# Optimization experiments

Measured on AMD Instinct MI355X. Metric: run time of the kernel, lower is better.

## Reference

```python
import jax, jax.numpy as jnp
import numpy as np

B, H, W = 256, 256, 256
MIN_ = 100          # bg seeds sampled per image
MAX_ = 100          # fg seeds sampled per image
MIN_P = 0.1         # fraction of lowest-cam pixels forming bg candidate pool
FG_ERODE_K = 11
FG_ERODE_ITER = 1
KSZ = 3             # dilation kernel
IGNORE = -255


def setup_inputs() -> dict:
    key = jax.random.key(0)
    x = jax.random.uniform(key, (B, 1, H, W), dtype=jnp.float32)  # CAMs in [0,1)
    return {"x": x}


def _minpool(m, k):
    # kornia-style binary erosion with ones kernel == min-pool, SAME padding
    return jax.lax.reduce_window(m, jnp.inf, jax.lax.min, (1, k, k), (1, 1, 1), 'SAME')


def _maxpool(m, k):
    # kornia-style binary dilation with ones kernel == max-pool, SAME padding
    return jax.lax.reduce_window(m, -jnp.inf, jax.lax.max, (1, k, k), (1, 1, 1), 'SAME')


def _otsu(hist):
    # hist: (b,256) float32; returns per-sample Otsu threshold in [0,255]
    bc = jnp.arange(256, dtype=jnp.float32)
    w1 = jnp.cumsum(hist, -1)
    total = w1[:, -1:]
    w2 = total - w1 + hist                      # reverse cumulative weight
    s1 = jnp.cumsum(hist * bc, -1)
    s2 = s1[:, -1:] - s1 + hist * bc
    m1 = s1 / jnp.maximum(w1, 1.0)
    m2 = s2 / jnp.maximum(w2, 1.0)
    var12 = w1[:, :-1] * w2[:, 1:] * (m1[:, :-1] - m2[:, 1:]) ** 2
    return bc[jnp.argmax(var12, axis=-1)]        # (b,)


def reference(x):
    b, _, h, w = x.shape
    hw = h * w
    cam = x[:, 0]                                # (b,h,w)
    cam255 = jnp.floor(cam * 255.0)
    ci = jnp.clip(cam255, 0, 255).astype(jnp.int32).reshape(b, hw)

    hist = jax.vmap(lambda v: jnp.bincount(v, length=256))(ci).astype(jnp.float32)
    th = _otsu(hist)                              # (b,)
    th = jnp.where(th <= 0.0, 1.0, jnp.where(th >= 255.0, 254.0, th))
    bad = (ci.max(-1) == ci.min(-1))              # degenerate CAM -> no seeds

    # ----- fg: threshold, erode, uniform sample w/o replacement (Gumbel top-k) -----
    roi = (cam255 > th[:, None, None]).astype(jnp.float32)
    for _ in range(FG_ERODE_ITER):
        roi = _minpool(roi, FG_ERODE_K)
    roi_f = roi.reshape(b, hw)

    key = jax.random.key(42)
    kf, kb = jax.random.split(key)
    neg = jnp.float32(-jnp.inf)
    rows = jnp.arange(b)[:, None]

    sc_fg = jnp.where(roi_f > 0, jax.random.uniform(kf, (b, hw)), neg)
    v_fg, i_fg = jax.lax.top_k(sc_fg, MAX_)       # picks min(MAX_, n_fg) pixels
    fg = jnp.zeros((b, hw), jnp.float32).at[rows, i_fg].set(
        jnp.isfinite(v_fg).astype(jnp.float32))

    # ----- bg: lowest nbr_bg cam pixels are candidates; sample MIN_ of them -----
    nbr_bg = int(MIN_P * h * w)
    order = jnp.argsort(cam.reshape(b, hw), axis=-1)  # ascending
    cand = jnp.zeros((b, hw), jnp.float32).at[rows, order[:, :nbr_bg]].set(1.0)
    sc_bg = jnp.where(cand > 0, jax.random.uniform(kb, (b, hw)), neg)
    v_bg, i_bg = jax.lax.top_k(sc_bg, MIN_)
    bg = jnp.zeros((b, hw), jnp.float32).at[rows, i_bg].set(
        jnp.isfinite(v_bg).astype(jnp.float32))

    keep = (~bad)[:, None].astype(jnp.float32)
    fg = (fg * keep).reshape(b, h, w)
    bg = (bg * keep).reshape(b, h, w)

    # ----- dilate seeds, drop conflicts, assemble label map -----
    fg = _maxpool(fg, KSZ)
    bg = _maxpool(bg, KSZ)
    conflict = (fg + bg) >= 2.0
    fg = jnp.where(conflict, 0.0, fg)
    bg = jnp.where(conflict, 0.0, bg)

    out = jnp.full((b, h, w), IGNORE, jnp.int32)
    out = jnp.where(fg == 1.0, 1, out)
    out = jnp.where(bg == 1.0, 0, out)
    return out
```

## Files before the change

kernel.cpp:

```cpp
#include <hip/hip_runtime.h>
#include <stdint.h>

#define PARTITIONABLE 1

typedef unsigned int u32;
typedef unsigned long long u64;
typedef __attribute__((ext_vector_type(4))) int int4v;

static constexpr int BB  = 256;
static constexpr int HWN = 65536;
static constexpr u32 K_BG = 6553;
static constexpr u32 TOPK = 100;
static constexpr u32 CAP  = 7936;
static constexpr u32 FG_CAP = 1024;

static constexpr int OFF_LST   = 0;
static constexpr int OFF_FVL   = 0;
static constexpr int OFF_BVL   = 8192;
static constexpr int OFF_FHL   = 16384;
static constexpr int OFF_BHL   = 24576;
static constexpr int OFF_CIMG  = 63488;
static constexpr int OFF_FGL   = 63488;
static constexpr int OFF_SEEDB = 71680;
static constexpr int OFF_SEEDF = 79872;
static constexpr int OFF_HIST  = 129024;
static constexpr int OFF_HROWS = 137216;
static constexpr int OFF_ROWS  = 145408;
static constexpr int OFF_HO    = 153600;
static constexpr int OFF_EQ    = 154624;
static constexpr int OFF_SCAL  = 155648;
static constexpr int ARENA_BYTES = 155776;

__host__ __device__ inline u32 rotl32(u32 x, int d) { return (x << d) | (x >> (32 - d)); }

#define TF_ROUND(r) do { x0 += x1; x1 = rotl32(x1, r); x1 ^= x0; } while (0)

__host__ __device__ inline void threefry2x32(u32 k0, u32 k1, u32 x0, u32 x1, u32& o0, u32& o1) {
  u32 ks2 = k0 ^ k1 ^ 0x1BD11BDAu;
  x0 += k0; x1 += k1;
  TF_ROUND(13); TF_ROUND(15); TF_ROUND(26); TF_ROUND(6);
  x0 += k1;  x1 += ks2 + 1u;
  TF_ROUND(17); TF_ROUND(29); TF_ROUND(16); TF_ROUND(24);
  x0 += ks2; x1 += k0 + 2u;
  TF_ROUND(13); TF_ROUND(15); TF_ROUND(26); TF_ROUND(6);
  x0 += k0;  x1 += k1 + 3u;
  TF_ROUND(17); TF_ROUND(29); TF_ROUND(16); TF_ROUND(24);
  x0 += k1;  x1 += ks2 + 4u;
  TF_ROUND(13); TF_ROUND(15); TF_ROUND(26); TF_ROUND(6);
  x0 += ks2; x1 += k0 + 5u;
  o0 = x0; o1 = x1;
}

__device__ inline u32 score_bits(u32 k0, u32 k1, u32 i) {
#if PARTITIONABLE
  u32 a, b;
  threefry2x32(k0, k1, 0u, i, a, b);
  return a ^ b;
#else
  const u32 HALF = 1u << 23;
  u32 a, b;
  if (i < HALF) { threefry2x32(k0, k1, i, i + HALF, a, b); return a; }
  threefry2x32(k0, k1, i - HALF, i, a, b); return b;
#endif
}

__device__ __forceinline__ u32 wscan_incl(u32 v, int lane) {
#pragma unroll
  for (int d = 1; d < 64; d <<= 1) { u32 t = __shfl_up(v, d, 64); if (lane >= d) v += t; }
  return v;
}

template<int BPT, int NT>
__device__ __forceinline__ void pselA(const u32* hist, u32* ws, int t, u32* h, u32& loc, u32& inc) {
  int lane = t & 63;
  loc = 0;
#pragma unroll
  for (int j = 0; j < BPT; j++) { h[j] = hist[BPT * t + j]; loc += h[j]; }
  inc = wscan_incl(loc, lane);
  if (lane == 63) ws[t >> 6] = inc;
}
template<int BPT, int NT>
__device__ __forceinline__ void pselB(u32 K, bool desc, const u32* ws, u32* sc, int t, const u32* h, u32 loc, u32 inc) {
  const int NW = NT / 64;
  int wid = t >> 6;
  u32 off = 0, total = 0;
#pragma unroll
  for (int k = 0; k < NW; k++) { u32 wv = ws[k]; total += wv; if (k < wid) off += wv; }
  inc += off;
  if (!desc) {
    u32 ex = inc - loc;
#pragma unroll
    for (int j = 0; j < BPT; j++) { if (ex < K && K <= ex + h[j]) { sc[0] = BPT * t + j; sc[1] = K - ex; } ex += h[j]; }
  } else {
    u32 ex = total - inc;
#pragma unroll
    for (int j = BPT - 1; j >= 0; j--) { if (ex < K && K <= ex + h[j]) { sc[0] = BPT * t + j; sc[1] = K - ex; } ex += h[j]; }
  }
}

template<int BPT, int NT>
__device__ void psel_full(u32* hist, u32 K, bool desc, u32* ws, u32* sc, int zeroN, int tid) {
  u32 h[BPT], loc = 0, inc = 0;
  bool act = tid < NT;
  if (act) pselA<BPT, NT>(hist, ws, tid, h, loc, inc);
  __syncthreads();
  if (act) pselB<BPT, NT>(K, desc, ws, sc, tid, h, loc, inc);
  for (int k = tid; k < zeroN; k += 1024) hist[k] = 0;
  __syncthreads();
}

__device__ __forceinline__ void otsu_wave0(const u32* hO, u32* scal, int lane) {
  u32 base = (u32)lane * 4;
  u32 h[4], cw[4], cs[4];
#pragma unroll
  for (int j = 0; j < 4; j++) h[j] = hO[base + j];
  cw[0] = h[0]; cs[0] = h[0] * base;
#pragma unroll
  for (int j = 1; j < 4; j++) { cw[j] = cw[j-1] + h[j]; cs[j] = cs[j-1] + h[j] * (base + j); }
  u32 incW = wscan_incl(cw[3], lane);
  u32 incS = wscan_incl(cs[3], lane);
  u32 offW = incW - cw[3], offS = incS - cs[3];
  u32 totW = __shfl(incW, 63, 64), totS = __shfl(incS, 63, 64);
  int nz = 0;
#pragma unroll
  for (int j = 0; j < 4; j++) nz += (h[j] != 0);
#pragma unroll
  for (int d = 1; d < 64; d <<= 1) nz += __shfl_xor(nz, d, 64);
  u32 selfW0 = cw[0] + offW, selfS0 = cs[0] + offS;
  u32 nxtW = __shfl_down(selfW0, 1, 64);
  u32 nxtS = __shfl_down(selfS0, 1, 64);
  u32 nxtH = __shfl_down(h[0], 1, 64);
  float total = (float)totW, stot = (float)totS;
  unsigned long long best = 0ull;
#pragma unroll
  for (int j = 0; j < 4; j++) {
    int t = (int)base + j;
    if (t < 255) {
      float h1 = (float)((j < 3) ? h[j+1] : nxtH);
      float w1 = (float)(cw[j] + offW);
      float w1n = (j < 3) ? (float)(cw[j+1] + offW) : (float)nxtW;
      float s1 = (float)(cs[j] + offS);
      float s1n = (j < 3) ? (float)(cs[j+1] + offS) : (float)nxtS;
      float w2 = total - w1n + h1;
      float s2 = stot - s1n + h1 * (float)(t + 1);
      float m1 = s1 / fmaxf(w1, 1.0f);
      float m2 = s2 / fmaxf(w2, 1.0f);
      float d = m1 - m2;
      float v = (w1 * w2) * (d * d);
      unsigned long long key = ((unsigned long long)__float_as_uint(v) << 32) | (u32)(255 - t);
      if (key > best) best = key;
    }
  }
#pragma unroll
  for (int d = 1; d < 64; d <<= 1) { unsigned long long o = __shfl_xor(best, d, 64); if (o > best) best = o; }
  if (lane == 0) {
    int bi = 255 - (int)(best & 0xFFFFFFFFu);
    float th = (float)bi;
    th = (th <= 0.0f) ? 1.0f : ((th >= 255.0f) ? 254.0f : th);
    scal[8] = (u32)(int)th;
    scal[5] = (nz <= 1) ? 1u : 0u;
  }
}

__device__ __forceinline__ void roi_bits(const u32* cImgW, u64* rows, u32 thiU, int tid) {
  u64 bits = 0;
#pragma unroll
  for (int k2 = 0; k2 < 16; k2++) {
    int k = (k2 + (tid >> 1)) & 15;
    u32 v4 = cImgW[tid * 16 + k];
    u32 m = 0;
    if ((v4 & 0xFFu) > thiU)         m |= 1u;
    if (((v4 >> 8) & 0xFFu) > thiU)  m |= 2u;
    if (((v4 >> 16) & 0xFFu) > thiU) m |= 4u;
    if ((v4 >> 24) > thiU)           m |= 8u;
    bits |= (u64)m << (4 * k);
  }
  rows[tid] = bits;
}

__device__ __forceinline__ void erode_h(const u64* rows, u64* hrows, int r) {
  u64 wv[4], h0[4];
  for (int j = 0; j < 4; j++) { wv[j] = rows[r * 4 + j]; h0[j] = wv[j]; }
  for (int s = 1; s <= 5; s++)
    for (int j = 0; j < 4; j++) {
      u64 hi = (j < 3) ? wv[j + 1] : ~0ull;
      u64 lo = (j > 0) ? wv[j - 1] : ~0ull;
      h0[j] &= ((wv[j] >> s) | (hi << (64 - s))) & ((wv[j] << s) | (lo >> (64 - s)));
    }
  for (int j = 0; j < 4; j++) hrows[r * 4 + j] = h0[j];
}

__device__ __forceinline__ void erode_v(const u64* hrows, u64* rows, int r) {
  u64 res[4] = {hrows[r * 4], hrows[r * 4 + 1], hrows[r * 4 + 2], hrows[r * 4 + 3]};
  for (int dr = -5; dr <= 5; dr++) {
    if (dr == 0) continue;
    int rr = r + dr;
    if (rr < 0 || rr >= 256) continue;
    for (int j = 0; j < 4; j++) res[j] &= hrows[rr * 4 + j];
  }
  for (int j = 0; j < 4; j++) rows[r * 4 + j] = res[j];
}

__device__ void seed_generic(u64* lst2, u32 n, u32 k0, u32 k1, u32 bimg, u64* seedRows,
                             u32* hist, u32* eqA, u32* scal, u32* ws, bool dead, int tid) {
  u32* sc = scal + 2;
  seedRows[tid] = 0;
  for (u32 e = tid; e < n; e += 1024) {
    u32 idx = (u32)(lst2[e] & 0xFFFFu);
    u32 m = score_bits(k0, k1, (bimg << 16) | idx) >> 9;
    lst2[e] = ((u64)m << 16) | idx;
    atomicAdd(&hist[m >> 12], 1u);
  }
  if (tid == 0) scal[1] = 0;
  __syncthreads();
  u32 keff = n < TOPK ? n : TOPK;
  psel_full<2, 1024>(hist, keff, true, ws, sc, 4096, tid);
  u32 s0 = sc[0], Kr = sc[1];
  for (u32 e = tid; e < n; e += 1024) { u32 m = (u32)(lst2[e] >> 16); if ((m >> 12) == s0) atomicAdd(&hist[m & 0xFFFu], 1u); }
  __syncthreads();
  psel_full<4, 1024>(hist, Kr, true, ws, sc, 2048, tid);
  u32 S = (s0 << 12) | sc[0]; u32 tiesS = sc[1];
  for (u32 e = tid; e < n; e += 1024) {
    u64 le = lst2[e]; u32 m = (u32)(le >> 16); u32 idx = (u32)(le & 0xFFFFu);
    if (m > S) { if (!dead) atomicOr(&seedRows[idx >> 6], 1ull << (idx & 63)); }
    else if (m == S) { u32 p = atomicAdd(&scal[1], 1u); if (p < 256) eqA[p] = idx; }
  }
  __syncthreads();
  if (tid == 0) {
    u32 ne = scal[1] < 256u ? scal[1] : 256u;
    for (u32 i2 = 1; i2 < ne; i2++) { u32 v = eqA[i2]; int j = (int)i2 - 1; while (j >= 0 && eqA[j] > v) { eqA[j + 1] = eqA[j]; j--; } eqA[j + 1] = v; }
    scal[4] = ne;
  }
  __syncthreads();
  { u32 ne = scal[4]; u32 tk = tiesS < ne ? tiesS : ne;
    if (!dead && (u32)tid < tk) { u32 idx = eqA[tid]; atomicOr(&seedRows[idx >> 6], 1ull << (idx & 63)); } }
  __syncthreads();
}

__global__ __launch_bounds__(1024, 4) void k_all(const float* __restrict__ x,
                                                 u32 kf0, u32 kf1, u32 kb0, u32 kb1,
                                                 int* __restrict__ out) {
  __shared__ __align__(16) char arena[ARENA_BYTES];
  const int b = blockIdx.x, tid = threadIdx.x;
  const int lane = tid & 63;

  u64* lst    = (u64*)(arena + OFF_LST);
  u32* cImgW  = (u32*)(arena + OFF_CIMG);
  u32* hO     = (u32*)(arena + OFF_HO);
  u32* hist   = (u32*)(arena + OFF_HIST);
  u32* eqA    = (u32*)(arena + OFF_EQ);
  u32* scal   = (u32*)(arena + OFF_SCAL);
  u32* ws     = scal + 10;
  u32* sc     = scal + 2;
  u64* rows   = (u64*)(arena + OFF_ROWS);
  u64* hrows  = (u64*)(arena + OFF_HROWS);
  u64* fgList = (u64*)(arena + OFF_FGL);
  u64* seedB  = (u64*)(arena + OFF_SEEDB);
  u64* seedF  = (u64*)(arena + OFF_SEEDF);

  const u32 BND = __float_as_uint(0.110f);
  const float4* img4 = (const float4*)(x + (size_t)b * HWN);
  const float* img = x + (size_t)b * HWN;

  if (tid < 256) hO[tid] = 0;
  hist[tid] = 0; hist[tid + 1024] = 0;
  if (tid < 10) scal[tid] = 0;
  __syncthreads();

#pragma unroll
  for (int half = 0; half < 2; ++half) {
    float4 v[8];
#pragma unroll
    for (int k = 0; k < 8; k++) v[k] = img4[((half * 8 + k) << 10) + tid];
    u32 nq = 0;
#pragma unroll
    for (int k = 0; k < 8; k++) {
      u32 c0 = (u32)(int)(v[k].x * 255.0f);
      u32 c1 = (u32)(int)(v[k].y * 255.0f);
      u32 c2 = (u32)(int)(v[k].z * 255.0f);
      u32 c3 = (u32)(int)(v[k].w * 255.0f);
      atomicAdd(&hO[c0], 1u); atomicAdd(&hO[c1], 1u);
      atomicAdd(&hO[c2], 1u); atomicAdd(&hO[c3], 1u);
      cImgW[((half * 8 + k) << 10) + tid] = c0 | (c1 << 8) | (c2 << 16) | (c3 << 24);
      u32 q0 = __float_as_uint(v[k].x), q1 = __float_as_uint(v[k].y);
      u32 q2 = __float_as_uint(v[k].z), q3 = __float_as_uint(v[k].w);
      if (q0 < BND) { nq++; atomicAdd(&hist[q0 >> 19], 1u); }
      if (q1 < BND) { nq++; atomicAdd(&hist[q1 >> 19], 1u); }
      if (q2 < BND) { nq++; atomicAdd(&hist[q2 >> 19], 1u); }
      if (q3 < BND) { nq++; atomicAdd(&hist[q3 >> 19], 1u); }
    }
    u32 incl = wscan_incl(nq, lane);
    u32 wtot = __shfl(incl, 63, 64);
    u32 base = 0;
    if (lane == 0) base = atomicAdd(&scal[0], wtot);
    base = __shfl(base, 0, 64);
    u32 pos = base + incl - nq;
#pragma unroll
    for (int k = 0; k < 8; k++) {
      u32 q0 = __float_as_uint(v[k].x), q1 = __float_as_uint(v[k].y);
      u32 q2 = __float_as_uint(v[k].z), q3 = __float_as_uint(v[k].w);
      u32 pix = (u32)((((half * 8 + k) << 10) + tid) * 4);
      if (q0 < BND) { if (pos < CAP) lst[pos] = ((u64)q0 << 16) | pix; pos++; }
      if (q1 < BND) { if (pos < CAP) lst[pos] = ((u64)q1 << 16) | (pix + 1); pos++; }
      if (q2 < BND) { if (pos < CAP) lst[pos] = ((u64)q2 << 16) | (pix + 2); pos++; }
      if (q3 < BND) { if (pos < CAP) lst[pos] = ((u64)q3 << 16) | (pix + 3); pos++; }
    }
  }
  __syncthreads();
  u32 cntBelow = scal[0];
  bool fastOK = (cntBelow >= K_BG && cntBelow <= CAP);

  {
    u32 h1v[4], loc1 = 0, inc1 = 0;
    if (tid < 64) otsu_wave0(hO, scal, lane);
    if (tid >= 512) pselA<4, 512>(hist, ws, tid - 512, h1v, loc1, inc1);
    __syncthreads();
    if (tid >= 512) pselB<4, 512>(K_BG, false, ws, sc, tid - 512, h1v, loc1, inc1);
    else { hist[tid*4] = 0; hist[tid*4+1] = 0; hist[tid*4+2] = 0; hist[tid*4+3] = 0; }
    __syncthreads();
  }
  u32 thiU = scal[8];
  bool dead = scal[5] != 0u;

  u32 T, listN;
  if (fastOK) {
    listN = cntBelow;
    u32 cb0 = sc[0], Kb = sc[1];
    for (u32 e = tid; e < listN; e += 1024) { u32 q = (u32)(lst[e] >> 16); if ((q >> 19) == cb0) atomicAdd(&hist[(q >> 8) & 0x7FFu], 1u); }
    roi_bits(cImgW, rows, thiU, tid);
    __syncthreads();
    u32 h2v[4], loc2 = 0, inc2 = 0;
    if (tid < 512) pselA<4, 512>(hist, ws, tid, h2v, loc2, inc2);
    __syncthreads();
    if (tid < 512) pselB<4, 512>(Kb, false, ws, sc, tid, h2v, loc2, inc2);
    else if (tid < 768) erode_h(rows, hrows, tid - 512);
    else hist[tid - 768] = 0;
    __syncthreads();
    u32 cb1 = sc[0], Kc = sc[1];
    u32 hi22 = (cb0 << 11) | cb1;
    for (u32 e = tid; e < listN; e += 1024) { u32 q = (u32)(lst[e] >> 16); if ((q >> 8) == hi22) atomicAdd(&hist[q & 0xFFu], 1u); }
    __syncthreads();
    u32 h3v[1], loc3 = 0, inc3 = 0;
    if (tid < 256) pselA<1, 256>(hist, ws, tid, h3v, loc3, inc3);
    else if (tid < 512) erode_v(hrows, rows, tid - 256);
    __syncthreads();
    if (tid < 256) pselB<1, 256>(Kc, false, ws, sc, tid, h3v, loc3, inc3);
    else if (tid >= 512) { int t0 = tid - 512; hist[t0*4] = 0; hist[t0*4+1] = 0; hist[t0*4+2] = 0; hist[t0*4+3] = 0; }
    __syncthreads();
    T = (hi22 << 8) | sc[0];
    u32 tiesCam = sc[1];
    for (u32 e = tid; e < listN; e += 1024) {
      u64 le = lst[e];
      if ((u32)(le >> 16) == T) { u32 p = atomicAdd(&scal[1], 1u); if (p < 256) eqA[p] = (u32)(le & 0xFFFFu); }
    }
    { u64 wv = rows[tid];
      while (wv) { int bit = __ffsll((long long)wv) - 1; wv &= wv - 1; u32 p = atomicAdd(&scal[7], 1u); if (p < FG_CAP) fgList[p] = (u64)(u32)(tid * 64 + bit); } }
    __syncthreads();
    if (tid == 0) {
      u32 ne = scal[1] < 256u ? scal[1] : 256u;
      for (u32 i2 = 1; i2 < ne; i2++) { u32 v = eqA[i2]; int j = (int)i2 - 1; while (j >= 0 && eqA[j] > v) { eqA[j + 1] = eqA[j]; j--; } eqA[j + 1] = v; }
      scal[9] = (tiesCam > 0 && tiesCam <= ne) ? eqA[tiesCam - 1] : ((tiesCam > 0) ? 0xFFFFFFFEu : 0xFFFFFFFFu);
    }
    __syncthreads();
  } else {
    for (int k2 = tid; k2 < 4096; k2 += 1024) hist[k2] = 0;
    __syncthreads();
    for (int c = 0; c < 64; c++) atomicAdd(&hist[__float_as_uint(img[(c << 10) + tid]) >> 19], 1u);
    __syncthreads();
    psel_full<2, 1024>(hist, K_BG, false, ws, sc, 2048, tid);
    u32 cb0 = sc[0], Kb = sc[1];
    if (tid == 0) scal[0] = 0;
    __syncthreads();
    for (int c = 0; c < 64; c++) {
      int i = (c << 10) + tid; u32 q = __float_as_uint(img[i]);
      if ((q >> 19) == cb0) { u32 p = atomicAdd(&scal[0], 1u); if (p < CAP) lst[p] = ((u64)q << 16) | (u32)i; }
    }
    __syncthreads();
    u32 ln = scal[0] < CAP ? scal[0] : CAP;
    for (u32 e = tid; e < ln; e += 1024) { u32 q = (u32)(lst[e] >> 16); atomicAdd(&hist[(q >> 8) & 0x7FFu], 1u); }
    __syncthreads();
    psel_full<2, 1024>(hist, Kb, false, ws, sc, 256, tid);
    u32 cb1 = sc[0], Kc = sc[1];
    u32 hi22 = (cb0 << 11) | cb1;
    for (u32 e = tid; e < ln; e += 1024) { u32 q = (u32)(lst[e] >> 16); if ((q >> 8) == hi22) atomicAdd(&hist[q & 0xFFu], 1u); }
    __syncthreads();
    psel_full<1, 256>(hist, Kc, false, ws, sc, 2048, tid);
    T = (hi22 << 8) | sc[0];
    u32 tiesCam = sc[1];
    if (tid == 0) scal[1] = 0;
    __syncthreads();
    for (u32 e = tid; e < ln; e += 1024) {
      u64 le = lst[e];
      if ((u32)(le >> 16) == T) { u32 p = atomicAdd(&scal[1], 1u); if (p < 256) eqA[p] = (u32)(le & 0xFFFFu); }
    }
    __syncthreads();
    if (tid == 0) {
      u32 ne = scal[1] < 256u ? scal[1] : 256u;
      for (u32 i2 = 1; i2 < ne; i2++) { u32 v = eqA[i2]; int j = (int)i2 - 1; while (j >= 0 && eqA[j] > v) { eqA[j + 1] = eqA[j]; j--; } eqA[j + 1] = v; }
      scal[9] = (tiesCam > 0 && tiesCam <= ne) ? eqA[tiesCam - 1] : ((tiesCam > 0) ? 0xFFFFFFFEu : 0xFFFFFFFFu);
      scal[0] = 0;
    }
    __syncthreads();
    u32 tmaxF = scal[9];
    for (int c = 0; c < 64; c++) {
      int i = (c << 10) + tid; u32 q = __float_as_uint(img[i]);
      bool sel = (q < T) || (q == T && tmaxF != 0xFFFFFFFFu && (u32)i <= tmaxF);
      if (sel) { u32 p = atomicAdd(&scal[0], 1u); if (p < CAP) lst[p] = ((u64)q << 16) | (u32)i; }
    }
    roi_bits(cImgW, rows, thiU, tid);
    __syncthreads();
    if (tid < 256) erode_h(rows, hrows, tid);
    __syncthreads();
    if (tid < 256) erode_v(hrows, rows, tid);
    __syncthreads();
    { u64 wv = rows[tid];
      while (wv) { int bit = __ffsll((long long)wv) - 1; wv &= wv - 1; u32 p = atomicAdd(&scal[7], 1u); if (p < FG_CAP) fgList[p] = (u64)(u32)(tid * 64 + bit); } }
    __syncthreads();
    listN = scal[0] < CAP ? scal[0] : CAP;
  }

  u32 camTmaxU = scal[9];
  u32 fgN = scal[7] < FG_CAP ? scal[7] : FG_CAP;
  if (fgN > 0) seed_generic(fgList, fgN, kf0, kf1, (u32)b, seedF, hist, eqA, scal, ws, dead, tid);

  u64 mine[8]; int nm = 0;
  for (u32 e = tid; e < listN; e += 1024) {
    u64 le = lst[e]; u32 q = (u32)(le >> 16); u32 idx = (u32)(le & 0xFFFFu);
    if (q < T || (q == T && camTmaxU != 0xFFFFFFFFu && idx <= camTmaxU)) { if (nm < 8) mine[nm++] = le; }
  }
  if (tid == 0) { scal[1] = 0; scal[6] = 0; }
  __syncthreads();
  {
    u32 nmU = (u32)nm;
    u32 incl = wscan_incl(nmU, lane);
    u32 wtot = __shfl(incl, 63, 64);
    u32 base2 = 0;
    if (lane == 0) base2 = atomicAdd(&scal[6], wtot);
    base2 = __shfl(base2, 0, 64);
    u32 my = base2 + incl - nmU;
    for (int k2 = 0; k2 < nm; k2++) {
      u32 idx = (u32)(mine[k2] & 0xFFFFu);
      u32 m = score_bits(kb0, kb1, ((u32)b << 16) | idx) >> 9;
      if (my + (u32)k2 < CAP) lst[my + k2] = ((u64)m << 16) | idx;
      atomicAdd(&hist[m >> 12], 1u);
    }
    seedB[tid] = 0;
    if (fgN == 0) seedF[tid] = 0;
  }
  __syncthreads();
  u32 candN = scal[6] < CAP ? scal[6] : CAP;
  u32 keff = candN < TOPK ? candN : TOPK;

  if (keff > 0) {
    u32 hb1[2], locb1 = 0, incb1 = 0;
    pselA<2, 1024>(hist, ws, tid, hb1, locb1, incb1);
    __syncthreads();
    pselB<2, 1024>(keff, true, ws, sc, tid, hb1, locb1, incb1);
    for (int k2 = tid; k2 < 4096; k2 += 1024) hist[k2] = 0;
    __syncthreads();
    u32 s0b = sc[0], Krb = sc[1];
    for (u32 e = tid; e < candN; e += 1024) { u32 m = (u32)(lst[e] >> 16); if ((m >> 12) == s0b) atomicAdd(&hist[m & 0xFFFu], 1u); }
    __syncthreads();
    u32 hb2[4], locb2 = 0, incb2 = 0;
    pselA<4, 1024>(hist, ws, tid, hb2, locb2, incb2);
    __syncthreads();
    pselB<4, 1024>(Krb, true, ws, sc, tid, hb2, locb2, incb2);
    __syncthreads();
    u32 S = (s0b << 12) | sc[0]; u32 tiesS = sc[1];
    for (u32 e = tid; e < candN; e += 1024) {
      u64 le = lst[e]; u32 m = (u32)(le >> 16); u32 idx = (u32)(le & 0xFFFFu);
      if (m > S) { if (!dead) atomicOr(&seedB[idx >> 6], 1ull << (idx & 63)); }
      else if (m == S) { u32 p = atomicAdd(&scal[1], 1u); if (p < 256) eqA[p] = idx; }
    }
    __syncthreads();
    if (tid == 0) {
      u32 ne = scal[1] < 256u ? scal[1] : 256u;
      for (u32 i2 = 1; i2 < ne; i2++) { u32 v = eqA[i2]; int j = (int)i2 - 1; while (j >= 0 && eqA[j] > v) { eqA[j + 1] = eqA[j]; j--; } eqA[j + 1] = v; }
      scal[4] = ne;
    }
    __syncthreads();
    { u32 ne = scal[4]; u32 tk = tiesS < ne ? tiesS : ne;
      if (!dead && (u32)tid < tk) { u32 idx = eqA[tid]; atomicOr(&seedB[idx >> 6], 1ull << (idx & 63)); } }
    __syncthreads();
  }

  u64* fvL = (u64*)(arena + OFF_FVL);
  u64* bvL = (u64*)(arena + OFF_BVL);
  u64* fhL = (u64*)(arena + OFF_FHL);
  u64* bhL = (u64*)(arena + OFF_BHL);
  {
    int r = tid >> 2;
    u64 vf = seedF[tid], vb = seedB[tid];
    if (r > 0)   { vf |= seedF[tid - 4]; vb |= seedB[tid - 4]; }
    if (r < 255) { vf |= seedF[tid + 4]; vb |= seedB[tid + 4]; }
    fvL[tid] = vf; bvL[tid] = vb;
  }
  __syncthreads();
  {
    int j = tid & 3;
    u64 v = fvL[tid];
    u64 L = (j > 0) ? fvL[tid - 1] : 0ull;
    u64 R = (j < 3) ? fvL[tid + 1] : 0ull;
    fhL[tid] = v | (v << 1) | (L >> 63) | (v >> 1) | (R << 63);
    v = bvL[tid];
    L = (j > 0) ? bvL[tid - 1] : 0ull;
    R = (j < 3) ? bvL[tid + 1] : 0ull;
    bhL[tid] = v | (v << 1) | (L >> 63) | (v >> 1) | (R << 63);
  }
  __syncthreads();
  int4v* out4 = (int4v*)(out + (size_t)b * HWN);
  for (int it = 0; it < 16; it++) {
    int idx4 = it * 1024 + tid;
    int word = idx4 >> 4;
    int sh = (idx4 & 15) * 4;
    u32 fb = (u32)(fhL[word] >> sh) & 0xFu;
    u32 gb = (u32)(bhL[word] >> sh) & 0xFu;
    u32 e = fb ^ gb;
    int4v o;
    o.x = (e & 1u)        ? (int)(fb & 1u)        : -255;
    o.y = ((e >> 1) & 1u) ? (int)((fb >> 1) & 1u) : -255;
    o.z = ((e >> 2) & 1u) ? (int)((fb >> 2) & 1u) : -255;
    o.w = ((e >> 3) & 1u) ? (int)((fb >> 3) & 1u) : -255;
    __builtin_nontemporal_store(o, out4 + idx4);
  }
}

extern "C" void kernel_launch(void* const* d_in, const int* in_sizes, int n_in,
                              void* d_out, int out_size, void* d_ws, size_t ws_size,
                              hipStream_t stream) {
  const float* x = (const float*)d_in[0];
  int* out = (int*)d_out;

  u32 kf0, kf1, kb0, kb1;
#if PARTITIONABLE
  threefry2x32(0u, 42u, 0u, 0u, kf0, kf1);
  threefry2x32(0u, 42u, 0u, 1u, kb0, kb1);
#else
  u32 a0, a1, c0, c1;
  threefry2x32(0u, 42u, 0u, 2u, a0, a1);
  threefry2x32(0u, 42u, 1u, 3u, c0, c1);
  kf0 = a0; kf1 = c0; kb0 = a1; kb1 = c1;
#endif

  k_all<<<BB, 1024, 0, stream>>>(x, kf0, kf1, kb0, kb1, out);
}
```

Baseline: 54.94 us.

## Replace final radix-select passes with small in-bin sort for bg threshold and seeds

In the fast path, the third histogram radix pass for the bg cam threshold is replaced: entries in the final 22-bit bin are collected with their low 8 bits into a small array, sorted by one thread, and the Kth entry gives threshold and tie index directly. For bg seed sampling, a single 4096-bin pass (11-bit shift) replaces two passes; the in-bin candidates are collected, sorted by (descending low bits, index), and the Kth key becomes the cutoff. Erosion work is moved to overlap earlier phases and histogram clearing is folded into existing steps. This removes several barriers and histogram passes, but relies on the final bin holding at most 256 entries and adds serial insertion-sort work on one thread.

```diff
diff --git a/kernel.cpp b/kernel.cpp
--- a/kernel.cpp
+++ b/kernel.cpp
@@ -218,7 +218,7 @@
   u32 s0 = sc[0], Kr = sc[1];
   for (u32 e = tid; e < n; e += 1024) { u32 m = (u32)(lst2[e] >> 16); if ((m >> 12) == s0) atomicAdd(&hist[m & 0xFFFu], 1u); }
   __syncthreads();
-  psel_full<4, 1024>(hist, Kr, true, ws, sc, 2048, tid);
+  psel_full<4, 1024>(hist, Kr, true, ws, sc, 4096, tid);
   u32 S = (s0 << 12) | sc[0]; u32 tiesS = sc[1];
   for (u32 e = tid; e < n; e += 1024) {
     u64 le = lst2[e]; u32 m = (u32)(le >> 16); u32 idx = (u32)(le & 0xFFFFu);
@@ -322,7 +322,7 @@
   u32 thiU = scal[8];
   bool dead = scal[5] != 0u;
 
-  u32 T, listN;
+  u32 listN;
   if (fastOK) {
     listN = cntBelow;
     u32 cb0 = sc[0], Kb = sc[1];
@@ -331,35 +331,27 @@
     __syncthreads();
     u32 h2v[4], loc2 = 0, inc2 = 0;
     if (tid < 512) pselA<4, 512>(hist, ws, tid, h2v, loc2, inc2);
+    else if (tid < 768) erode_h(rows, hrows, tid - 512);
     __syncthreads();
     if (tid < 512) pselB<4, 512>(Kb, false, ws, sc, tid, h2v, loc2, inc2);
-    else if (tid < 768) erode_h(rows, hrows, tid - 512);
-    else hist[tid - 768] = 0;
+    else if (tid < 768) erode_v(hrows, rows, tid - 512);
     __syncthreads();
     u32 cb1 = sc[0], Kc = sc[1];
     u32 hi22 = (cb0 << 11) | cb1;
-    for (u32 e = tid; e < listN; e += 1024) { u32 q = (u32)(lst[e] >> 16); if ((q >> 8) == hi22) atomicAdd(&hist[q & 0xFFu], 1u); }
-    __syncthreads();
-    u32 h3v[1], loc3 = 0, inc3 = 0;
-    if (tid < 256) pselA<1, 256>(hist, ws, tid, h3v, loc3, inc3);
-    else if (tid < 512) erode_v(hrows, rows, tid - 256);
-    __syncthreads();
-    if (tid < 256) pselB<1, 256>(Kc, false, ws, sc, tid, h3v, loc3, inc3);
-    else if (tid >= 512) { int t0 = tid - 512; hist[t0*4] = 0; hist[t0*4+1] = 0; hist[t0*4+2] = 0; hist[t0*4+3] = 0; }
-    __syncthreads();
-    T = (hi22 << 8) | sc[0];
-    u32 tiesCam = sc[1];
     for (u32 e = tid; e < listN; e += 1024) {
-      u64 le = lst[e];
-      if ((u32)(le >> 16) == T) { u32 p = atomicAdd(&scal[1], 1u); if (p < 256) eqA[p] = (u32)(le & 0xFFFFu); }
+      u64 le = lst[e]; u32 q = (u32)(le >> 16);
+      if ((q >> 8) == hi22) { u32 p = atomicAdd(&scal[1], 1u); if (p < 256) eqA[p] = ((q & 0xFFu) << 16) | (u32)(le & 0xFFFFu); }
     }
     { u64 wv = rows[tid];
       while (wv) { int bit = __ffsll((long long)wv) - 1; wv &= wv - 1; u32 p = atomicAdd(&scal[7], 1u); if (p < FG_CAP) fgList[p] = (u64)(u32)(tid * 64 + bit); } }
+    hist[tid] = 0; hist[tid + 1024] = 0; hist[tid + 2048] = 0; hist[tid + 3072] = 0;
     __syncthreads();
     if (tid == 0) {
       u32 ne = scal[1] < 256u ? scal[1] : 256u;
       for (u32 i2 = 1; i2 < ne; i2++) { u32 v = eqA[i2]; int j = (int)i2 - 1; while (j >= 0 && eqA[j] > v) { eqA[j + 1] = eqA[j]; j--; } eqA[j + 1] = v; }
-      scal[9] = (tiesCam > 0 && tiesCam <= ne) ? eqA[tiesCam - 1] : ((tiesCam > 0) ? 0xFFFFFFFEu : 0xFFFFFFFFu);
+      u32 ent = eqA[Kc - 1];
+      scal[26] = (hi22 << 8) | (ent >> 16);
+      scal[27] = ent & 0xFFFFu;
     }
     __syncthreads();
   } else {
@@ -385,26 +377,29 @@
     for (u32 e = tid; e < ln; e += 1024) { u32 q = (u32)(lst[e] >> 16); if ((q >> 8) == hi22) atomicAdd(&hist[q & 0xFFu], 1u); }
     __syncthreads();
     psel_full<1, 256>(hist, Kc, false, ws, sc, 2048, tid);
-    T = (hi22 << 8) | sc[0];
+    u32 T0 = (hi22 << 8) | sc[0];
     u32 tiesCam = sc[1];
     if (tid == 0) scal[1] = 0;
     __syncthreads();
     for (u32 e = tid; e < ln; e += 1024) {
       u64 le = lst[e];
-      if ((u32)(le >> 16) == T) { u32 p = atomicAdd(&scal[1], 1u); if (p < 256) eqA[p] = (u32)(le & 0xFFFFu); }
+      if ((u32)(le >> 16) == T0) { u32 p = atomicAdd(&scal[1], 1u); if (p < 256) eqA[p] = (u32)(le & 0xFFFFu); }
     }
     __syncthreads();
     if (tid == 0) {
       u32 ne = scal[1] < 256u ? scal[1] : 256u;
       for (u32 i2 = 1; i2 < ne; i2++) { u32 v = eqA[i2]; int j = (int)i2 - 1; while (j >= 0 && eqA[j] > v) { eqA[j + 1] = eqA[j]; j--; } eqA[j + 1] = v; }
-      scal[9] = (tiesCam > 0 && tiesCam <= ne) ? eqA[tiesCam - 1] : ((tiesCam > 0) ? 0xFFFFFFFEu : 0xFFFFFFFFu);
+      u32 tmF = (tiesCam > 0 && tiesCam <= ne) ? eqA[tiesCam - 1] : ((tiesCam > 0) ? 0xFFFFFFFEu : 0xFFFFFFFFu);
+      scal[9] = tmF;
+      scal[26] = T0;
+      scal[27] = tmF;
       scal[0] = 0;
     }
     __syncthreads();
     u32 tmaxF = scal[9];
     for (int c = 0; c < 64; c++) {
       int i = (c << 10) + tid; u32 q = __float_as_uint(img[i]);
-      bool sel = (q < T) || (q == T && tmaxF != 0xFFFFFFFFu && (u32)i <= tmaxF);
+      bool sel = (q < T0) || (q == T0 && tmaxF != 0xFFFFFFFFu && (u32)i <= tmaxF);
       if (sel) { u32 p = atomicAdd(&scal[0], 1u); if (p < CAP) lst[p] = ((u64)q << 16) | (u32)i; }
     }
     roi_bits(cImgW, rows, thiU, tid);
@@ -415,18 +410,20 @@
     __syncthreads();
     { u64 wv = rows[tid];
       while (wv) { int bit = __ffsll((long long)wv) - 1; wv &= wv - 1; u32 p = atomicAdd(&scal[7], 1u); if (p < FG_CAP) fgList[p] = (u64)(u32)(tid * 64 + bit); } }
+    hist[tid + 2048] = 0; hist[tid + 3072] = 0;
     __syncthreads();
     listN = scal[0] < CAP ? scal[0] : CAP;
   }
 
-  u32 camTmaxU = scal[9];
+  u32 T = scal[26];
+  u32 camTmax = scal[27];
   u32 fgN = scal[7] < FG_CAP ? scal[7] : FG_CAP;
   if (fgN > 0) seed_generic(fgList, fgN, kf0, kf1, (u32)b, seedF, hist, eqA, scal, ws, dead, tid);
 
   u64 mine[8]; int nm = 0;
   for (u32 e = tid; e < listN; e += 1024) {
     u64 le = lst[e]; u32 q = (u32)(le >> 16); u32 idx = (u32)(le & 0xFFFFu);
-    if (q < T || (q == T && camTmaxU != 0xFFFFFFFFu && idx <= camTmaxU)) { if (nm < 8) mine[nm++] = le; }
+    if (q < T || (q == T && idx <= camTmax)) { if (nm < 8) mine[nm++] = le; }
   }
   if (tid == 0) { scal[1] = 0; scal[6] = 0; }
   __syncthreads();
@@ -442,7 +439,7 @@
       u32 idx = (u32)(mine[k2] & 0xFFFFu);
       u32 m = score_bits(kb0, kb1, ((u32)b << 16) | idx) >> 9;
       if (my + (u32)k2 < CAP) lst[my + k2] = ((u64)m << 16) | idx;
-      atomicAdd(&hist[m >> 12], 1u);
+      atomicAdd(&hist[m >> 11], 1u);
     }
     seedB[tid] = 0;
     if (fgN == 0) seedF[tid] = 0;
@@ -452,35 +449,36 @@
   u32 keff = candN < TOPK ? candN : TOPK;
 
   if (keff > 0) {
-    u32 hb1[2], locb1 = 0, incb1 = 0;
-    pselA<2, 1024>(hist, ws, tid, hb1, locb1, incb1);
-    __syncthreads();
-    pselB<2, 1024>(keff, true, ws, sc, tid, hb1, locb1, incb1);
-    for (int k2 = tid; k2 < 4096; k2 += 1024) hist[k2] = 0;
-    __syncthreads();
-    u32 s0b = sc[0], Krb = sc[1];
-    for (u32 e = tid; e < candN; e += 1024) { u32 m = (u32)(lst[e] >> 16); if ((m >> 12) == s0b) atomicAdd(&hist[m & 0xFFFu], 1u); }
-    __syncthreads();
-    u32 hb2[4], locb2 = 0, incb2 = 0;
-    pselA<4, 1024>(hist, ws, tid, hb2, locb2, incb2);
-    __syncthreads();
-    pselB<4, 1024>(Krb, true, ws, sc, tid, hb2, locb2, incb2);
-    __syncthreads();
-    u32 S = (s0b << 12) | sc[0]; u32 tiesS = sc[1];
+    u32 hb1[4], locb1 = 0, incb1 = 0;
+    pselA<4, 1024>(hist, ws, tid, hb1, locb1, incb1);
+    __syncthreads();
+    pselB<4, 1024>(keff, true, ws, sc, tid, hb1, locb1, incb1);
+    __syncthreads();
+    u32 binB = sc[0], Krb = sc[1];
     for (u32 e = tid; e < candN; e += 1024) {
-      u64 le = lst[e]; u32 m = (u32)(le >> 16); u32 idx = (u32)(le & 0xFFFFu);
-      if (m > S) { if (!dead) atomicOr(&seedB[idx >> 6], 1ull << (idx & 63)); }
-      else if (m == S) { u32 p = atomicAdd(&scal[1], 1u); if (p < 256) eqA[p] = idx; }
+      u64 le = lst[e]; u32 m = (u32)(le >> 16);
+      if ((m >> 11) == binB) {
+        u32 k2 = ((0x7FFu - (m & 0x7FFu)) << 16) | (u32)(le & 0xFFFFu);
+        u32 p = atomicAdd(&scal[1], 1u); if (p < 256) eqA[p] = k2;
+      }
     }
     __syncthreads();
     if (tid == 0) {
       u32 ne = scal[1] < 256u ? scal[1] : 256u;
       for (u32 i2 = 1; i2 < ne; i2++) { u32 v = eqA[i2]; int j = (int)i2 - 1; while (j >= 0 && eqA[j] > v) { eqA[j + 1] = eqA[j]; j--; } eqA[j + 1] = v; }
-      scal[4] = ne;
-    }
-    __syncthreads();
-    { u32 ne = scal[4]; u32 tk = tiesS < ne ? tiesS : ne;
-      if (!dead && (u32)tid < tk) { u32 idx = eqA[tid]; atomicOr(&seedB[idx >> 6], 1ull << (idx & 63)); } }
+      scal[26] = eqA[Krb - 1];
+    }
+    __syncthreads();
+    u32 key2K = scal[26];
+    if (!dead) {
+      for (u32 e = tid; e < candN; e += 1024) {
+        u64 le = lst[e]; u32 m = (u32)(le >> 16); u32 idx = (u32)(le & 0xFFFFu);
+        u32 hb = m >> 11;
+        u32 k2 = ((0x7FFu - (m & 0x7FFu)) << 16) | idx;
+        bool sel = (hb > binB) || (hb == binB && k2 <= key2K);
+        if (sel) atomicOr(&seedB[idx >> 6], 1ull << (idx & 63));
+      }
+    }
     __syncthreads();
   }
 
```

Result: faster. 48.68 us (-11.4%).
